# Performance work log

Measured on AMD Instinct MI355X. Metric: run time of the kernel, lower is better.

## Reference

```python
import jax, jax.numpy as jnp
import numpy as np

HEADS = 4
GROUPS = 32
EPS = 1e-5


def setup_inputs() -> dict:
    key = jax.random.key(0)
    ks = jax.random.split(key, 3)
    B, C, H, W = 8, 256, 32, 32
    x = jax.random.normal(ks[0], (B, C, H, W), dtype=jnp.float32)
    gamma = jnp.ones((C,), jnp.float32)
    beta = jnp.zeros((C,), jnp.float32)
    w_qkv = jax.random.normal(ks[1], (3 * C, C), jnp.float32) * (1.0 / np.sqrt(C))
    b_qkv = jnp.zeros((3 * C,), jnp.float32)
    w_proj = jax.random.normal(ks[2], (C, C), jnp.float32) * (1.0 / np.sqrt(C))
    b_proj = jnp.zeros((C,), jnp.float32)
    return {"x": x, "gamma": gamma, "beta": beta, "w_qkv": w_qkv,
            "b_qkv": b_qkv, "w_proj": w_proj, "b_proj": b_proj}


def group_norm(x, gamma, beta):
    B, C, H, W = x.shape
    xg = x.reshape(B, GROUPS, C // GROUPS, H, W)
    mean = xg.mean(axis=(2, 3, 4), keepdims=True)
    var = xg.var(axis=(2, 3, 4), keepdims=True)
    xg = (xg - mean) * jax.lax.rsqrt(var + EPS)
    xn = xg.reshape(B, C, H, W)
    return xn * gamma[None, :, None, None] + beta[None, :, None, None]


def reference(x, gamma, beta, w_qkv, b_qkv, w_proj, b_proj):
    B, C, H, W = x.shape
    hd = C // HEADS  # head dim
    h = group_norm(x, gamma, beta)
    # 1x1 conv == channel matmul: [B,3C,H,W]
    qkv = jnp.einsum('oc,bchw->bohw', w_qkv, h) + b_qkv[None, :, None, None]
    qkv = qkv.reshape(B, 3, HEADS, hd, H * W)
    q, k, v = qkv[:, 0], qkv[:, 1], qkv[:, 2]  # each [B, heads, hd, HW]
    attn = jnp.einsum('bhci,bhcj->bhij', q, k) * (hd ** -0.5)
    attn = jax.nn.softmax(attn, axis=-1)
    out = jnp.einsum('bhij,bhcj->bhci', attn, v).reshape(B, C, H, W)
    proj = jnp.einsum('oc,bchw->bohw', w_proj, out) + b_proj[None, :, None, None]
    return x + proj
```

## Files before the change

kernel.cpp:

```cpp
#include <hip/hip_runtime.h>
#include <hip/hip_bf16.h>

static constexpr int kC = 256;
static constexpr int kN = 1024;

using s16x8 = __attribute__((ext_vector_type(8))) short;
using f32x4 = __attribute__((ext_vector_type(4))) float;
using u32x4 = __attribute__((ext_vector_type(4))) unsigned int;

__device__ inline f32x4 mfma16(s16x8 a, s16x8 b, f32x4 c) {
  return __builtin_amdgcn_mfma_f32_16x16x32_bf16(a, b, c, 0, 0, 0);
}

__device__ inline unsigned short f2bf(float f) {
  unsigned u = __builtin_bit_cast(unsigned, f);
  u = (u + 0x7fffu + ((u >> 16) & 1u)) >> 16;
  return (unsigned short)u;
}

__device__ inline float exp2_fast(float x) {
  float r;
  asm("v_exp_f32 %0, %1" : "=v"(r) : "v"(x));
  return r;
}

__device__ inline unsigned cvt_pk_bf16(float lo, float hi) {
  unsigned r;
  asm("v_cvt_pk_bf16_f32 %0, %1, %2" : "=v"(r) : "v"(lo), "v"(hi));
  return r;
}

static constexpr float kQScale = 0.18033688011112042f;

__global__ __launch_bounds__(256) void prep_kernel(
    const float* __restrict__ x, const float* __restrict__ gamma,
    const float* __restrict__ beta, unsigned short* __restrict__ hTp,
    const float* __restrict__ wq, const float* __restrict__ wp,
    unsigned short* __restrict__ Wqp, unsigned short* __restrict__ Wpp) {
  if (blockIdx.x < 128) {
    const int tid = blockIdx.x * 256 + threadIdx.x;
    const float* src;
    unsigned short* dst;
    if (tid < 24576) {
      const int fragid = tid >> 6, lane = tid & 63;
      const int Mt = fragid >> 3, kt = fragid & 7;
      src = wq + (size_t)(Mt * 16 + (lane & 15)) * 256 + kt * 32 + (lane >> 4) * 8;
      dst = Wqp + (size_t)tid * 8;
    } else {
      const int id = tid - 24576;
      const int fragid = id >> 6, lane = id & 63;
      const int Mt = fragid >> 3, kt = fragid & 7;
      src = wp + (size_t)(Mt * 16 + (lane & 15)) * 256 + kt * 32 + (lane >> 4) * 8;
      dst = Wpp + (size_t)id * 8;
    }
    const float4 f0 = *(const float4*)src;
    const float4 f1 = *(const float4*)(src + 4);
    ushort4 o0, o1;
    o0.x = f2bf(f0.x); o0.y = f2bf(f0.y); o0.z = f2bf(f0.z); o0.w = f2bf(f0.w);
    o1.x = f2bf(f1.x); o1.y = f2bf(f1.y); o1.z = f2bf(f1.z); o1.w = f2bf(f1.w);
    *(ushort4*)dst = o0;
    *(ushort4*)(dst + 4) = o1;
    return;
  }

  const int bg = blockIdx.x - 128;
  const int b = bg & 7, g = bg >> 3;
  const size_t base = ((size_t)b * kC + (size_t)g * 8) * kN;
  const float4* __restrict__ x4 = (const float4*)(x + base);
  const int t = threadIdx.x;

  float vv[8][4];
  float s = 0.f, ss = 0.f;
#pragma unroll
  for (int i = 0; i < 8; ++i) {
    const float4 v = x4[t + 256 * i];
    vv[i][0] = v.x; vv[i][1] = v.y; vv[i][2] = v.z; vv[i][3] = v.w;
    s += v.x + v.y + v.z + v.w;
    ss += v.x * v.x + v.y * v.y + v.z * v.z + v.w * v.w;
  }
#pragma unroll
  for (int off = 32; off > 0; off >>= 1) {
    s += __shfl_xor(s, off);
    ss += __shfl_xor(ss, off);
  }
  __shared__ float rs[4], rss[4];
  const int wave = t >> 6, lane = t & 63;
  if (lane == 0) { rs[wave] = s; rss[wave] = ss; }
  __syncthreads();
  s = rs[0] + rs[1] + rs[2] + rs[3];
  ss = rss[0] + rss[1] + rss[2] + rss[3];
  const float mean = s * (1.f / 8192.f);
  const float var = ss * (1.f / 8192.f) - mean * mean;
  const float rinv = rsqrtf(var + 1e-5f);
  float ga[8], be[8];
#pragma unroll
  for (int i = 0; i < 8; ++i) {
    ga[i] = gamma[g * 8 + i] * rinv;
    be[i] = beta[g * 8 + i] - mean * ga[i];
  }
  const int kt = g >> 2, gq = g & 3;
#pragma unroll
  for (int r = 0; r < 4; ++r) {
    const int pos = 4 * t + r;
    const int nt = pos >> 4, lp = pos & 15;
    unsigned short* dst =
        hTp + ((size_t)((b * 64 + nt) * 8 + kt) * 64 + (gq * 16 + lp)) * 8;
    ushort4 o0, o1;
    o0.x = f2bf(vv[0][r] * ga[0] + be[0]);
    o0.y = f2bf(vv[1][r] * ga[1] + be[1]);
    o0.z = f2bf(vv[2][r] * ga[2] + be[2]);
    o0.w = f2bf(vv[3][r] * ga[3] + be[3]);
    o1.x = f2bf(vv[4][r] * ga[4] + be[4]);
    o1.y = f2bf(vv[5][r] * ga[5] + be[5]);
    o1.z = f2bf(vv[6][r] * ga[6] + be[6]);
    o1.w = f2bf(vv[7][r] * ga[7] + be[7]);
    *(ushort4*)dst = o0;
    *(ushort4*)(dst + 4) = o1;
  }
}

__device__ inline void gload(const s16x8* __restrict__ Af,
                             const s16x8* __restrict__ Bf,
                             int Mt0, int Nt0, int kt, int lane,
                             s16x8 (&a)[4], s16x8 (&bb)[2]) {
#pragma unroll
  for (int mt = 0; mt < 4; ++mt)
    a[mt] = Af[((size_t)(Mt0 + mt) * 8 + kt) * 64 + lane];
#pragma unroll
  for (int nt = 0; nt < 2; ++nt)
    bb[nt] = Bf[((size_t)(Nt0 + nt) * 8 + kt) * 64 + lane];
}

__device__ inline void gmfma(const s16x8 (&a)[4], const s16x8 (&bb)[2],
                             f32x4 (&acc)[4][2], bool swap) {
  if (swap) {
#pragma unroll
    for (int mt = 0; mt < 4; ++mt)
#pragma unroll
      for (int nt = 0; nt < 2; ++nt)
        acc[mt][nt] = mfma16(bb[nt], a[mt], acc[mt][nt]);
  } else {
#pragma unroll
    for (int mt = 0; mt < 4; ++mt)
#pragma unroll
      for (int nt = 0; nt < 2; ++nt)
        acc[mt][nt] = mfma16(a[mt], bb[nt], acc[mt][nt]);
  }
}

__global__ __launch_bounds__(256) void gemm_qkv_kernel(
    const unsigned short* __restrict__ Wp, const float* __restrict__ bias,
    const unsigned short* __restrict__ Bp,
    unsigned short* __restrict__ Qp, unsigned short* __restrict__ Kp,
    unsigned short* __restrict__ Vp) {
  const int bid = blockIdx.x;
  const int swz = (bid & 7) * 96 + (bid >> 3);
  const int b = swz / 96, rr = swz % 96;
  const int mb = rr >> 4, nb = rr & 15;
  const int t = threadIdx.x;
  const int wave = t >> 6, lane = t & 63;
  const int li = lane & 15, grp = lane >> 4;
  const int m0 = mb * 128 + (wave >> 1) * 64;
  const int n0 = nb * 64 + (wave & 1) * 32;
  const bool swap = mb >= 4;
  const int Mt0 = m0 >> 4;
  const int Nt0 = b * 64 + (n0 >> 4);
  const s16x8* __restrict__ Af = (const s16x8*)Wp;
  const s16x8* __restrict__ Bf = (const s16x8*)Bp;

  f32x4 acc[4][2];
#pragma unroll
  for (int mt = 0; mt < 4; ++mt)
#pragma unroll
    for (int nt = 0; nt < 2; ++nt) acc[mt][nt] = f32x4{0.f, 0.f, 0.f, 0.f};

  s16x8 sa[3][4], sb[3][2];
  gload(Af, Bf, Mt0, Nt0, 0, lane, sa[0], sb[0]);
  gload(Af, Bf, Mt0, Nt0, 1, lane, sa[1], sb[1]);
#pragma unroll
  for (int kt = 0; kt < 8; ++kt) {
    if (kt + 2 < 8)
      gload(Af, Bf, Mt0, Nt0, kt + 2, lane, sa[(kt + 2) % 3], sb[(kt + 2) % 3]);
    gmfma(sa[kt % 3], sb[kt % 3], acc, swap);
  }

  if (!swap) {
    unsigned short* __restrict__ Tp = (mb < 2) ? Qp : Kp;
    const float qs = (mb < 2) ? kQScale : 1.0f;
#pragma unroll
    for (int mt = 0; mt < 4; ++mt) {
      const int mbase = m0 + mt * 16;
      const int head = (mbase >> 6) & 3;
      const int bh = b * 4 + head;
      const int c16 = mbase & 63;
      const int ks = c16 >> 5;
      const int grpp = ((c16 >> 3) + (grp >> 1)) & 3;
      const float4 bv = *(const float4*)(bias + mbase + 4 * grp);
#pragma unroll
      for (int nt = 0; nt < 2; ++nt) {
        const int pt = (n0 >> 4) + nt;
        ushort4 o;
        o.x = f2bf((acc[mt][nt][0] + bv.x) * qs);
        o.y = f2bf((acc[mt][nt][1] + bv.y) * qs);
        o.z = f2bf((acc[mt][nt][2] + bv.z) * qs);
        o.w = f2bf((acc[mt][nt][3] + bv.w) * qs);
        *(ushort4*)(Tp + (size_t)bh * 65536 +
                    ((size_t)(pt * 2 + ks) * 64 + grpp * 16 + li) * 8 +
                    (grp & 1) * 4) = o;
      }
    }
  } else {
#pragma unroll
    for (int mt = 0; mt < 4; ++mt) {
      const int mbase = m0 + mt * 16;
      const int head = (mbase >> 6) & 3;
      const int bh = b * 4 + head;
      const int ct = (mbase & 63) >> 4;
      const float bvc = bias[mbase + li];
      const int kvt = n0 >> 5;
#pragma unroll
      for (int nt = 0; nt < 2; ++nt) {
        ushort4 o;
        o.x = f2bf(acc[mt][nt][0] + bvc);
        o.y = f2bf(acc[mt][nt][1] + bvc);
        o.z = f2bf(acc[mt][nt][2] + bvc);
        o.w = f2bf(acc[mt][nt][3] + bvc);
        *(ushort4*)(Vp + (size_t)bh * 65536 +
                    ((size_t)(ct * 32 + kvt) * 64 + grp * 16 + li) * 8 +
                    nt * 4) = o;
      }
    }
  }
}

__global__ __launch_bounds__(512) void attn_proj_kernel(
    const unsigned short* __restrict__ Qp, const unsigned short* __restrict__ Kp,
    const unsigned short* __restrict__ Vp, const unsigned short* __restrict__ Wpp,
    const float* __restrict__ bpj, const float* __restrict__ x,
    float* __restrict__ out) {
  __shared__ __align__(16) unsigned short Ex[2][8][64][8];
  const int bid = blockIdx.x;
  const int swz = (bid & 7) * 32 + (bid >> 3);
  const int b = swz >> 5, qb = swz & 31;
  const int t = threadIdx.x;
  const int w8 = t >> 6, lane = t & 63;
  const int head = w8 & 3, qh = w8 >> 2;
  const int li = lane & 15, grp = lane >> 4;
  const int q0 = qb * 32 + qh * 16;
  const int bh = b * 4 + head;
  const unsigned short* __restrict__ Qb = Qp + (size_t)bh * 65536;
  const unsigned short* __restrict__ Kb = Kp + (size_t)bh * 65536;
  const unsigned short* __restrict__ Vb = Vp + (size_t)bh * 65536;

  s16x8 qf[2];
#pragma unroll
  for (int ks = 0; ks < 2; ++ks)
    qf[ks] = *(const s16x8*)(Qb + (((q0 >> 4) * 2 + ks) * 64 + lane) * 8);

  f32x4 O[4];
#pragma unroll
  for (int ct = 0; ct < 4; ++ct) O[ct] = f32x4{0.f, 0.f, 0.f, 0.f};
  f32x4 lvec = f32x4{0.f, 0.f, 0.f, 0.f};
  float m_run = -1.0e30f;

  auto loadK = [&](int it, s16x8 (&kk)[2][2]) {
#pragma unroll
    for (int mt = 0; mt < 2; ++mt)
#pragma unroll
      for (int ks = 0; ks < 2; ++ks)
        kk[mt][ks] = *(const s16x8*)(
            Kb + ((size_t)((it * 2 + mt) * 2 + ks) * 64 + lane) * 8);
  };
  auto loadV = [&](int it, s16x8 (&vv)[4]) {
#pragma unroll
    for (int ct = 0; ct < 4; ++ct)
      vv[ct] = *(const s16x8*)(Vb + ((size_t)(ct * 32 + it) * 64 + lane) * 8);
  };
  auto qkt = [&](const s16x8 (&kk)[2][2], f32x4 (&s)[2]) {
#pragma unroll
    for (int mt = 0; mt < 2; ++mt) {
      s[mt] = mfma16(kk[mt][0], qf[0], f32x4{0.f, 0.f, 0.f, 0.f});
      s[mt] = mfma16(kk[mt][1], qf[1], s[mt]);
    }
  };
  auto smaxpv = [&](f32x4 (&s)[2], const s16x8 (&vv)[4]) {
    const float A = fmaxf(fmaxf(s[0][0], s[0][1]), s[0][2]);
    const float B = fmaxf(fmaxf(s[0][3], s[1][0]), s[1][1]);
    const float C = fmaxf(fmaxf(s[1][2], s[1][3]), A);
    float pm = fmaxf(B, C);
    pm = fmaxf(pm, __shfl_xor(pm, 16));
    pm = fmaxf(pm, __shfl_xor(pm, 32));
    if (!__all(pm <= m_run + 8.0f)) {
      const float mnew = fmaxf(m_run, pm);
      const float f = exp2_fast(m_run - mnew);
      m_run = mnew;
      lvec *= f;
#pragma unroll
      for (int ct = 0; ct < 4; ++ct) O[ct] *= f;
    }
    f32x4 p[2];
#pragma unroll
    for (int mt = 0; mt < 2; ++mt) {
#pragma unroll
      for (int r = 0; r < 4; ++r) p[mt][r] = exp2_fast(s[mt][r] - m_run);
      lvec += p[mt];
    }
    u32x4 pk;
    pk[0] = cvt_pk_bf16(p[0][0], p[0][1]);
    pk[1] = cvt_pk_bf16(p[0][2], p[0][3]);
    pk[2] = cvt_pk_bf16(p[1][0], p[1][1]);
    pk[3] = cvt_pk_bf16(p[1][2], p[1][3]);
    const s16x8 pf = __builtin_bit_cast(s16x8, pk);
#pragma unroll
    for (int ct = 0; ct < 4; ++ct) O[ct] = mfma16(vv[ct], pf, O[ct]);
  };

  s16x8 k0[2][2], k1[2][2], v0[4], v1[4];
  loadK(0, k0);
  loadV(0, v0);
  f32x4 sc[2];
  qkt(k0, sc);
  loadK(1, k1);

#pragma unroll 1
  for (int h2 = 0; h2 < 16; ++h2) {
    const int tt = 2 * h2;
    loadV(tt + 1, v1);
    f32x4 sn[2];
    qkt(k1, sn);
    loadK(tt + 2, k0);
    smaxpv(sc, v0);
    loadV(tt + 2, v0);
    f32x4 s2[2];
    qkt(k0, s2);
    loadK(tt + 3, k1);
    smaxpv(sn, v1);
    sc[0] = s2[0];
    sc[1] = s2[1];
  }

  float lt = lvec[0] + lvec[1] + lvec[2] + lvec[3];
  lt += __shfl_xor(lt, 16);
  lt += __shfl_xor(lt, 32);
  const float rinv = 1.f / lt;
#pragma unroll
  for (int ct = 0; ct < 4; ++ct) {
    const int ktp = head * 2 + (ct >> 1);
    const int grpp = ((ct & 1) * 2 + (grp >> 1)) & 3;
    ushort4 o;
    o.x = f2bf(O[ct][0] * rinv);
    o.y = f2bf(O[ct][1] * rinv);
    o.z = f2bf(O[ct][2] * rinv);
    o.w = f2bf(O[ct][3] * rinv);
    *(ushort4*)&Ex[qh][ktp][grpp * 16 + li][(grp & 1) * 4] = o;
  }
  __syncthreads();

  {
    const int Mt0 = w8 * 2;
    const s16x8* __restrict__ Af = (const s16x8*)Wpp;
    f32x4 acc[2][2];
#pragma unroll
    for (int mt = 0; mt < 2; ++mt)
#pragma unroll
      for (int nt = 0; nt < 2; ++nt) acc[mt][nt] = f32x4{0.f, 0.f, 0.f, 0.f};

    s16x8 pa[3][2];
    auto loadA = [&](int kt, s16x8 (&a)[2]) {
#pragma unroll
      for (int mt = 0; mt < 2; ++mt)
        a[mt] = Af[((size_t)(Mt0 + mt) * 8 + kt) * 64 + lane];
    };
    loadA(0, pa[0]);
    loadA(1, pa[1]);
#pragma unroll
    for (int kt = 0; kt < 8; ++kt) {
      if (kt + 2 < 8) loadA(kt + 2, pa[(kt + 2) % 3]);
      s16x8 bb[2];
#pragma unroll
      for (int nt = 0; nt < 2; ++nt)
        bb[nt] = *(const s16x8*)&Ex[nt][kt][lane][0];
#pragma unroll
      for (int mt = 0; mt < 2; ++mt)
#pragma unroll
        for (int nt = 0; nt < 2; ++nt)
          acc[mt][nt] = mfma16(pa[kt % 3][mt], bb[nt], acc[mt][nt]);
    }

#pragma unroll
    for (int mt = 0; mt < 2; ++mt) {
      const int mbase = w8 * 32 + mt * 16 + 4 * grp;
      const float4 bv = *(const float4*)(bpj + mbase);
      const float bvr[4] = {bv.x, bv.y, bv.z, bv.w};
#pragma unroll
      for (int nt = 0; nt < 2; ++nt) {
        const int pos = qb * 32 + nt * 16 + li;
#pragma unroll
        for (int r2 = 0; r2 < 4; ++r2) {
          const size_t ob = ((size_t)(b * 256 + mbase + r2)) * 1024 + pos;
          out[ob] = acc[mt][nt][r2] + bvr[r2] + x[ob];
        }
      }
    }
  }
}

extern "C" void kernel_launch(void* const* d_in, const int* in_sizes, int n_in,
                              void* d_out, int out_size, void* d_ws, size_t ws_size,
                              hipStream_t stream) {
  const float* x      = (const float*)d_in[0];
  const float* gamma  = (const float*)d_in[1];
  const float* beta   = (const float*)d_in[2];
  const float* w_qkv  = (const float*)d_in[3];
  const float* b_qkv  = (const float*)d_in[4];
  const float* w_proj = (const float*)d_in[5];
  const float* b_proj = (const float*)d_in[6];
  float* out = (float*)d_out;

  unsigned short* ws = (unsigned short*)d_ws;
  unsigned short* Wqp  = ws;
  unsigned short* Wpp  = Wqp + 196608;
  unsigned short* hTp  = Wpp + 65536;
  unsigned short* Qp   = hTp + 2097152;
  unsigned short* Kp   = Qp + 2097152;
  unsigned short* Vp   = Kp + 2097152;

  hipLaunchKernelGGL(prep_kernel, dim3(384), dim3(256), 0, stream,
                     x, gamma, beta, hTp, w_qkv, w_proj, Wqp, Wpp);
  hipLaunchKernelGGL(gemm_qkv_kernel, dim3(768), dim3(256), 0, stream,
                     Wqp, b_qkv, hTp, Qp, Kp, Vp);
  hipLaunchKernelGGL(attn_proj_kernel, dim3(256), dim3(512), 0, stream,
                     Qp, Kp, Vp, Wpp, b_proj, x, out);
}
```

Baseline: 41.70 us.

## Fuse QKV GEMM and attention into one persistent kernel with per-batch counters

Merges the QKV GEMM and the attention+projection kernels into one 512-block kernel. Each block computes three 64x64 QKV tiles, then waits on an atomic per-batch counter until all 64 blocks of that batch are done, then runs attention for 16 queries across 4 heads. This removes one kernel launch and its tail, and lets batches start attention as soon as their own QKV is ready. In exchange it relies on all 512 blocks being co-resident (launch_bounds 256,2) to avoid deadlock, adds a memset, and adds s_setprio around the MFMA sections.

```diff
diff --git a/kernel.cpp b/kernel.cpp
--- a/kernel.cpp
+++ b/kernel.cpp
@@ -119,134 +119,141 @@
   }
 }
 
-__device__ inline void gload(const s16x8* __restrict__ Af,
-                             const s16x8* __restrict__ Bf,
-                             int Mt0, int Nt0, int kt, int lane,
-                             s16x8 (&a)[4], s16x8 (&bb)[2]) {
-#pragma unroll
-  for (int mt = 0; mt < 4; ++mt)
+__device__ inline void gload2(const s16x8* __restrict__ Af,
+                              const s16x8* __restrict__ Bf,
+                              int Mt0, int Nt0, int kt, int lane,
+                              s16x8 (&a)[2], s16x8 (&bb)[2]) {
+#pragma unroll
+  for (int mt = 0; mt < 2; ++mt)
     a[mt] = Af[((size_t)(Mt0 + mt) * 8 + kt) * 64 + lane];
 #pragma unroll
   for (int nt = 0; nt < 2; ++nt)
     bb[nt] = Bf[((size_t)(Nt0 + nt) * 8 + kt) * 64 + lane];
 }
 
-__device__ inline void gmfma(const s16x8 (&a)[4], const s16x8 (&bb)[2],
-                             f32x4 (&acc)[4][2], bool swap) {
+__device__ inline void gmfma2(const s16x8 (&a)[2], const s16x8 (&bb)[2],
+                              f32x4 (&acc)[2][2], bool swap) {
   if (swap) {
 #pragma unroll
-    for (int mt = 0; mt < 4; ++mt)
+    for (int mt = 0; mt < 2; ++mt)
 #pragma unroll
       for (int nt = 0; nt < 2; ++nt)
         acc[mt][nt] = mfma16(bb[nt], a[mt], acc[mt][nt]);
   } else {
 #pragma unroll
-    for (int mt = 0; mt < 4; ++mt)
+    for (int mt = 0; mt < 2; ++mt)
 #pragma unroll
       for (int nt = 0; nt < 2; ++nt)
         acc[mt][nt] = mfma16(a[mt], bb[nt], acc[mt][nt]);
   }
 }
 
-__global__ __launch_bounds__(256) void gemm_qkv_kernel(
-    const unsigned short* __restrict__ Wp, const float* __restrict__ bias,
-    const unsigned short* __restrict__ Bp,
+__global__ __launch_bounds__(256, 2) void fused_kernel(
+    const unsigned short* __restrict__ Wqp, const float* __restrict__ bq,
+    const unsigned short* __restrict__ hTp,
     unsigned short* __restrict__ Qp, unsigned short* __restrict__ Kp,
-    unsigned short* __restrict__ Vp) {
+    unsigned short* __restrict__ Vp,
+    const unsigned short* __restrict__ Wpp, const float* __restrict__ bpj,
+    const float* __restrict__ x, float* __restrict__ out,
+    unsigned* __restrict__ cnt) {
+  __shared__ __align__(16) unsigned short Ex[8][64][8];
   const int bid = blockIdx.x;
-  const int swz = (bid & 7) * 96 + (bid >> 3);
-  const int b = swz / 96, rr = swz % 96;
-  const int mb = rr >> 4, nb = rr & 15;
+  const int b = bid & 7;
+  const int u = bid >> 3;
   const int t = threadIdx.x;
   const int wave = t >> 6, lane = t & 63;
   const int li = lane & 15, grp = lane >> 4;
-  const int m0 = mb * 128 + (wave >> 1) * 64;
-  const int n0 = nb * 64 + (wave & 1) * 32;
-  const bool swap = mb >= 4;
-  const int Mt0 = m0 >> 4;
-  const int Nt0 = b * 64 + (n0 >> 4);
-  const s16x8* __restrict__ Af = (const s16x8*)Wp;
-  const s16x8* __restrict__ Bf = (const s16x8*)Bp;
-
-  f32x4 acc[4][2];
-#pragma unroll
-  for (int mt = 0; mt < 4; ++mt)
-#pragma unroll
-    for (int nt = 0; nt < 2; ++nt) acc[mt][nt] = f32x4{0.f, 0.f, 0.f, 0.f};
-
-  s16x8 sa[3][4], sb[3][2];
-  gload(Af, Bf, Mt0, Nt0, 0, lane, sa[0], sb[0]);
-  gload(Af, Bf, Mt0, Nt0, 1, lane, sa[1], sb[1]);
-#pragma unroll
-  for (int kt = 0; kt < 8; ++kt) {
-    if (kt + 2 < 8)
-      gload(Af, Bf, Mt0, Nt0, kt + 2, lane, sa[(kt + 2) % 3], sb[(kt + 2) % 3]);
-    gmfma(sa[kt % 3], sb[kt % 3], acc, swap);
-  }
-
-  if (!swap) {
-    unsigned short* __restrict__ Tp = (mb < 2) ? Qp : Kp;
-    const float qs = (mb < 2) ? kQScale : 1.0f;
-#pragma unroll
-    for (int mt = 0; mt < 4; ++mt) {
-      const int mbase = m0 + mt * 16;
-      const int head = (mbase >> 6) & 3;
-      const int bh = b * 4 + head;
-      const int c16 = mbase & 63;
-      const int ks = c16 >> 5;
-      const int grpp = ((c16 >> 3) + (grp >> 1)) & 3;
-      const float4 bv = *(const float4*)(bias + mbase + 4 * grp);
-#pragma unroll
-      for (int nt = 0; nt < 2; ++nt) {
-        const int pt = (n0 >> 4) + nt;
-        ushort4 o;
-        o.x = f2bf((acc[mt][nt][0] + bv.x) * qs);
-        o.y = f2bf((acc[mt][nt][1] + bv.y) * qs);
-        o.z = f2bf((acc[mt][nt][2] + bv.z) * qs);
-        o.w = f2bf((acc[mt][nt][3] + bv.w) * qs);
-        *(ushort4*)(Tp + (size_t)bh * 65536 +
-                    ((size_t)(pt * 2 + ks) * 64 + grpp * 16 + li) * 8 +
-                    (grp & 1) * 4) = o;
+  const int wm = wave >> 1, wn = wave & 1;
+
+  {
+    const s16x8* __restrict__ Af = (const s16x8*)Wqp;
+    const s16x8* __restrict__ Bf = (const s16x8*)hTp;
+#pragma unroll 1
+    for (int p = 0; p < 3; ++p) {
+      const int r = p * 64 + u;
+      const int mb = r >> 4, nb = r & 15;
+      const int m0 = mb * 64 + wm * 32;
+      const int n0 = nb * 64 + wn * 32;
+      const int Mt0 = m0 >> 4;
+      const int Nt0 = b * 64 + (n0 >> 4);
+      const bool swap = mb >= 8;
+      f32x4 acc[2][2];
+#pragma unroll
+      for (int mt = 0; mt < 2; ++mt)
+#pragma unroll
+        for (int nt = 0; nt < 2; ++nt) acc[mt][nt] = f32x4{0.f, 0.f, 0.f, 0.f};
+      s16x8 aA[2], bA[2], aB[2], bB[2];
+      gload2(Af, Bf, Mt0, Nt0, 0, lane, aA, bA);
+#pragma unroll
+      for (int kt = 0; kt < 8; kt += 2) {
+        gload2(Af, Bf, Mt0, Nt0, kt + 1, lane, aB, bB);
+        gmfma2(aA, bA, acc, swap);
+        if (kt + 2 < 8) gload2(Af, Bf, Mt0, Nt0, kt + 2, lane, aA, bA);
+        gmfma2(aB, bB, acc, swap);
       }
-    }
-  } else {
-#pragma unroll
-    for (int mt = 0; mt < 4; ++mt) {
-      const int mbase = m0 + mt * 16;
-      const int head = (mbase >> 6) & 3;
-      const int bh = b * 4 + head;
-      const int ct = (mbase & 63) >> 4;
-      const float bvc = bias[mbase + li];
-      const int kvt = n0 >> 5;
-#pragma unroll
-      for (int nt = 0; nt < 2; ++nt) {
-        ushort4 o;
-        o.x = f2bf(acc[mt][nt][0] + bvc);
-        o.y = f2bf(acc[mt][nt][1] + bvc);
-        o.z = f2bf(acc[mt][nt][2] + bvc);
-        o.w = f2bf(acc[mt][nt][3] + bvc);
-        *(ushort4*)(Vp + (size_t)bh * 65536 +
-                    ((size_t)(ct * 32 + kvt) * 64 + grp * 16 + li) * 8 +
-                    nt * 4) = o;
+
+      if (!swap) {
+        unsigned short* __restrict__ Tp = (mb < 4) ? Qp : Kp;
+        const float qs = (mb < 4) ? kQScale : 1.0f;
+#pragma unroll
+        for (int mt = 0; mt < 2; ++mt) {
+          const int mbase = m0 + mt * 16;
+          const int head = (mbase >> 6) & 3;
+          const int bh = b * 4 + head;
+          const int c16 = mbase & 63;
+          const int ks = c16 >> 5;
+          const int grpp = ((c16 >> 3) + (grp >> 1)) & 3;
+          const float4 bv = *(const float4*)(bq + mbase + 4 * grp);
+#pragma unroll
+          for (int nt = 0; nt < 2; ++nt) {
+            const int pt = (n0 >> 4) + nt;
+            ushort4 o;
+            o.x = f2bf((acc[mt][nt][0] + bv.x) * qs);
+            o.y = f2bf((acc[mt][nt][1] + bv.y) * qs);
+            o.z = f2bf((acc[mt][nt][2] + bv.z) * qs);
+            o.w = f2bf((acc[mt][nt][3] + bv.w) * qs);
+            *(ushort4*)(Tp + (size_t)bh * 65536 +
+                        ((size_t)(pt * 2 + ks) * 64 + grpp * 16 + li) * 8 +
+                        (grp & 1) * 4) = o;
+          }
+        }
+      } else {
+#pragma unroll
+        for (int mt = 0; mt < 2; ++mt) {
+          const int mbase = m0 + mt * 16;
+          const int head = (mbase >> 6) & 3;
+          const int bh = b * 4 + head;
+          const int ct = (mbase & 63) >> 4;
+          const float bvc = bq[mbase + li];
+          const int kvt = n0 >> 5;
+#pragma unroll
+          for (int nt = 0; nt < 2; ++nt) {
+            ushort4 o;
+            o.x = f2bf(acc[mt][nt][0] + bvc);
+            o.y = f2bf(acc[mt][nt][1] + bvc);
+            o.z = f2bf(acc[mt][nt][2] + bvc);
+            o.w = f2bf(acc[mt][nt][3] + bvc);
+            *(ushort4*)(Vp + (size_t)bh * 65536 +
+                        ((size_t)(ct * 32 + kvt) * 64 + grp * 16 + li) * 8 +
+                        nt * 4) = o;
+          }
+        }
       }
     }
   }
-}
-
-__global__ __launch_bounds__(512) void attn_proj_kernel(
-    const unsigned short* __restrict__ Qp, const unsigned short* __restrict__ Kp,
-    const unsigned short* __restrict__ Vp, const unsigned short* __restrict__ Wpp,
-    const float* __restrict__ bpj, const float* __restrict__ x,
-    float* __restrict__ out) {
-  __shared__ __align__(16) unsigned short Ex[2][8][64][8];
-  const int bid = blockIdx.x;
-  const int swz = (bid & 7) * 32 + (bid >> 3);
-  const int b = swz >> 5, qb = swz & 31;
-  const int t = threadIdx.x;
-  const int w8 = t >> 6, lane = t & 63;
-  const int head = w8 & 3, qh = w8 >> 2;
-  const int li = lane & 15, grp = lane >> 4;
-  const int q0 = qb * 32 + qh * 16;
+
+  __syncthreads();
+  if (t == 0) {
+    __hip_atomic_fetch_add(&cnt[b], 1u, __ATOMIC_RELAXED,
+                           __HIP_MEMORY_SCOPE_AGENT);
+    while (__hip_atomic_load(&cnt[b], __ATOMIC_RELAXED,
+                             __HIP_MEMORY_SCOPE_AGENT) < 64u)
+      __builtin_amdgcn_s_sleep(8);
+  }
+  __syncthreads();
+  __builtin_amdgcn_fence(__ATOMIC_ACQUIRE, "agent");
+
+  const int head = wave;
   const int bh = b * 4 + head;
   const unsigned short* __restrict__ Qb = Qp + (size_t)bh * 65536;
   const unsigned short* __restrict__ Kb = Kp + (size_t)bh * 65536;
@@ -255,7 +262,7 @@
   s16x8 qf[2];
 #pragma unroll
   for (int ks = 0; ks < 2; ++ks)
-    qf[ks] = *(const s16x8*)(Qb + (((q0 >> 4) * 2 + ks) * 64 + lane) * 8);
+    qf[ks] = *(const s16x8*)(Qb + ((u * 2 + ks) * 64 + lane) * 8);
 
   f32x4 O[4];
 #pragma unroll
@@ -277,11 +284,13 @@
       vv[ct] = *(const s16x8*)(Vb + ((size_t)(ct * 32 + it) * 64 + lane) * 8);
   };
   auto qkt = [&](const s16x8 (&kk)[2][2], f32x4 (&s)[2]) {
+    __builtin_amdgcn_s_setprio(1);
 #pragma unroll
     for (int mt = 0; mt < 2; ++mt) {
       s[mt] = mfma16(kk[mt][0], qf[0], f32x4{0.f, 0.f, 0.f, 0.f});
       s[mt] = mfma16(kk[mt][1], qf[1], s[mt]);
     }
+    __builtin_amdgcn_s_setprio(0);
   };
   auto smaxpv = [&](f32x4 (&s)[2], const s16x8 (&vv)[4]) {
     const float A = fmaxf(fmaxf(s[0][0], s[0][1]), s[0][2]);
@@ -311,32 +320,35 @@
     pk[2] = cvt_pk_bf16(p[1][0], p[1][1]);
     pk[3] = cvt_pk_bf16(p[1][2], p[1][3]);
     const s16x8 pf = __builtin_bit_cast(s16x8, pk);
+    __builtin_amdgcn_s_setprio(1);
 #pragma unroll
     for (int ct = 0; ct < 4; ++ct) O[ct] = mfma16(vv[ct], pf, O[ct]);
+    __builtin_amdgcn_s_setprio(0);
   };
 
-  s16x8 k0[2][2], k1[2][2], v0[4], v1[4];
-  loadK(0, k0);
-  loadV(0, v0);
-  f32x4 sc[2];
-  qkt(k0, sc);
-  loadK(1, k1);
-
+  {
+    s16x8 k0[2][2], k1[2][2], v0[4], v1[4];
+    loadK(0, k0);
+    loadV(0, v0);
+    f32x4 sc[2];
+    qkt(k0, sc);
+    loadK(1, k1);
 #pragma unroll 1
-  for (int h2 = 0; h2 < 16; ++h2) {
-    const int tt = 2 * h2;
-    loadV(tt + 1, v1);
-    f32x4 sn[2];
-    qkt(k1, sn);
-    loadK(tt + 2, k0);
-    smaxpv(sc, v0);
-    loadV(tt + 2, v0);
-    f32x4 s2[2];
-    qkt(k0, s2);
-    loadK(tt + 3, k1);
-    smaxpv(sn, v1);
-    sc[0] = s2[0];
-    sc[1] = s2[1];
+    for (int h2 = 0; h2 < 16; ++h2) {
+      const int tt = 2 * h2;
+      loadV(tt + 1, v1);
+      f32x4 sn[2];
+      qkt(k1, sn);
+      loadK(tt + 2, k0);
+      smaxpv(sc, v0);
+      loadV(tt + 2, v0);
+      f32x4 s2[2];
+      qkt(k0, s2);
+      loadK(tt + 3, k1);
+      smaxpv(sn, v1);
+      sc[0] = s2[0];
+      sc[1] = s2[1];
+    }
   }
 
   float lt = lvec[0] + lvec[1] + lvec[2] + lvec[3];
@@ -352,23 +364,21 @@
     o.y = f2bf(O[ct][1] * rinv);
     o.z = f2bf(O[ct][2] * rinv);
     o.w = f2bf(O[ct][3] * rinv);
-    *(ushort4*)&Ex[qh][ktp][grpp * 16 + li][(grp & 1) * 4] = o;
+    *(ushort4*)&Ex[ktp][grpp * 16 + li][(grp & 1) * 4] = o;
   }
   __syncthreads();
 
   {
-    const int Mt0 = w8 * 2;
+    const int Mt0 = wave * 4;
     const s16x8* __restrict__ Af = (const s16x8*)Wpp;
-    f32x4 acc[2][2];
-#pragma unroll
-    for (int mt = 0; mt < 2; ++mt)
-#pragma unroll
-      for (int nt = 0; nt < 2; ++nt) acc[mt][nt] = f32x4{0.f, 0.f, 0.f, 0.f};
-
-    s16x8 pa[3][2];
-    auto loadA = [&](int kt, s16x8 (&a)[2]) {
-#pragma unroll
-      for (int mt = 0; mt < 2; ++mt)
+    f32x4 acc[4];
+#pragma unroll
+    for (int mt = 0; mt < 4; ++mt) acc[mt] = f32x4{0.f, 0.f, 0.f, 0.f};
+
+    s16x8 pa[3][4];
+    auto loadA = [&](int kt, s16x8 (&a)[4]) {
+#pragma unroll
+      for (int mt = 0; mt < 4; ++mt)
         a[mt] = Af[((size_t)(Mt0 + mt) * 8 + kt) * 64 + lane];
     };
     loadA(0, pa[0]);
@@ -376,30 +386,22 @@
 #pragma unroll
     for (int kt = 0; kt < 8; ++kt) {
       if (kt + 2 < 8) loadA(kt + 2, pa[(kt + 2) % 3]);
-      s16x8 bb[2];
-#pragma unroll
-      for (int nt = 0; nt < 2; ++nt)
-        bb[nt] = *(const s16x8*)&Ex[nt][kt][lane][0];
-#pragma unroll
-      for (int mt = 0; mt < 2; ++mt)
-#pragma unroll
-        for (int nt = 0; nt < 2; ++nt)
-          acc[mt][nt] = mfma16(pa[kt % 3][mt], bb[nt], acc[mt][nt]);
-    }
-
-#pragma unroll
-    for (int mt = 0; mt < 2; ++mt) {
-      const int mbase = w8 * 32 + mt * 16 + 4 * grp;
+      const s16x8 bb = *(const s16x8*)&Ex[kt][lane][0];
+#pragma unroll
+      for (int mt = 0; mt < 4; ++mt)
+        acc[mt] = mfma16(pa[kt % 3][mt], bb, acc[mt]);
+    }
+
+#pragma unroll
+    for (int mt = 0; mt < 4; ++mt) {
+      const int mbase = wave * 64 + mt * 16 + 4 * grp;
       const float4 bv = *(const float4*)(bpj + mbase);
       const float bvr[4] = {bv.x, bv.y, bv.z, bv.w};
-#pragma unroll
-      for (int nt = 0; nt < 2; ++nt) {
-        const int pos = qb * 32 + nt * 16 + li;
-#pragma unroll
-        for (int r2 = 0; r2 < 4; ++r2) {
-          const size_t ob = ((size_t)(b * 256 + mbase + r2)) * 1024 + pos;
-          out[ob] = acc[mt][nt][r2] + bvr[r2] + x[ob];
-        }
+      const int pos = u * 16 + li;
+#pragma unroll
+      for (int r2 = 0; r2 < 4; ++r2) {
+        const size_t ob = ((size_t)(b * 256 + mbase + r2)) * 1024 + pos;
+        out[ob] = acc[mt][r2] + bvr[r2] + x[ob];
       }
     }
   }
@@ -424,11 +426,11 @@
   unsigned short* Qp   = hTp + 2097152;
   unsigned short* Kp   = Qp + 2097152;
   unsigned short* Vp   = Kp + 2097152;
-
+  unsigned* cnt = (unsigned*)(Vp + 2097152 + 1048576);
+
+  hipMemsetAsync(cnt, 0, 8 * sizeof(unsigned), stream);
   hipLaunchKernelGGL(prep_kernel, dim3(384), dim3(256), 0, stream,
                      x, gamma, beta, hTp, w_qkv, w_proj, Wqp, Wpp);
-  hipLaunchKernelGGL(gemm_qkv_kernel, dim3(768), dim3(256), 0, stream,
-                     Wqp, b_qkv, hTp, Qp, Kp, Vp);
-  hipLaunchKernelGGL(attn_proj_kernel, dim3(256), dim3(512), 0, stream,
-                     Qp, Kp, Vp, Wpp, b_proj, x, out);
-}
+  hipLaunchKernelGGL(fused_kernel, dim3(512), dim3(256), 0, stream,
+                     Wqp, b_qkv, hTp, Qp, Kp, Vp, Wpp, b_proj, x, out, cnt);
+}
```

Measured after the change: 74.36 us. 1.78x slower.
